# Performance work log

Measured on AMD Instinct MI355X. Metric: run time of the kernel, lower is better.

## Reference

```python
import jax, jax.numpy as jnp
import numpy as np

ALPHA = 0.2  # LeakyReLU negative slope
MASK_VAL = -1e9


def setup_inputs() -> dict:
    key = jax.random.key(0)
    k1, k2, k3, k4 = jax.random.split(key, 4)
    B, N, F_in, F_out = 8, 2048, 512, 512
    h = jax.random.normal(k1, (B, N, F_in), dtype=jnp.float32)
    adj = jax.random.randint(k2, (B, N, N), 0, 2, dtype=jnp.int32)
    # xavier_uniform with gain=1.414
    def xavier(k, shape, gain=1.414):
        fan_in, fan_out = shape[0], shape[1]
        bound = gain * np.sqrt(6.0 / (fan_in + fan_out))
        return jax.random.uniform(k, shape, jnp.float32, -bound, bound)
    W = xavier(k3, (F_in, F_out))
    a = xavier(k4, (2 * F_out, 1))
    return {"h": h, "adj": adj, "W": W, "a": a}


def reference(h, adj, W, a):
    # h: [B,N,Fin], adj: [B,N,N], W: [Fin,Fout], a: [2*Fout,1]
    Fout = W.shape[1]
    Wh = jnp.matmul(h, W)  # [B,N,Fout]
    # Split 'a' into source/target halves: concat([Wh_i, Wh_j]) @ a
    #   == (Wh_i @ a1) + (Wh_j @ a2), avoiding the O(N^2*2F) concat tensor.
    a1 = a[:Fout, 0]   # [Fout]
    a2 = a[Fout:, 0]   # [Fout]
    e_i = jnp.einsum('bnf,f->bn', Wh, a1)  # [B,N] score contribution of node i
    e_j = jnp.einsum('bnf,f->bn', Wh, a2)  # [B,N] score contribution of node j
    e = e_i[:, :, None] + e_j[:, None, :]  # [B,N,N]
    e = jax.nn.leaky_relu(e, negative_slope=ALPHA)
    e = jnp.where(adj == 0, MASK_VAL, e)
    attention = jax.nn.softmax(e, axis=2)  # [B,N,N]
    h_prime = jnp.matmul(attention, Wh)    # [B,N,Fout]
    return jax.nn.elu(h_prime)
```

## Files before the change

### kernel.cpp

```cpp
#include <hip/hip_runtime.h>
#include <hip/hip_bf16.h>

#define ALPHA 0.2f
#define LOG2E 1.44269504088896340736f

typedef float  f32x4 __attribute__((ext_vector_type(4)));
typedef float  f32x2 __attribute__((ext_vector_type(2)));
typedef int    i32x4 __attribute__((ext_vector_type(4)));
typedef int    i32x2 __attribute__((ext_vector_type(2)));

static __device__ __forceinline__ void mfma_bf16_16x16x32(f32x4& c, i32x4 a, i32x4 b) {
  asm("v_mfma_f32_16x16x32_bf16 %0, %1, %2, %0" : "+v"(c) : "v"(a), "v"(b));
}

static __device__ __forceinline__ unsigned short f2bf(float x) {
  __hip_bfloat16 b = __float2bfloat16(x);
  return *reinterpret_cast<unsigned short*>(&b);
}
static __device__ __forceinline__ unsigned int packbf2(float x, float y) {
  return (unsigned int)f2bf(x) | ((unsigned int)f2bf(y) << 16);
}
static __device__ __forceinline__ float dot4(f32x4 a, f32x4 b) {
  return a.x*b.x + a.y*b.y + a.z*b.z + a.w*b.w;
}

__global__ __launch_bounds__(256) void k_setup(const float* __restrict__ W, const float* __restrict__ a,
                                               unsigned short* __restrict__ wt,
                                               float* __restrict__ v1, float* __restrict__ v2) {
  const int bid = blockIdx.x, tid = threadIdx.x;
  __shared__ float S[32][33];
  if (bid < 256) {
    const int k0 = (bid >> 4) * 32, f0 = (bid & 15) * 32;
    const int r = tid >> 5, c = tid & 31;
    #pragma unroll
    for (int rr = r; rr < 32; rr += 8) S[rr][c] = W[(size_t)(k0 + rr) * 512 + f0 + c];
    __syncthreads();
    #pragma unroll
    for (int rr = r; rr < 32; rr += 8) wt[(size_t)(f0 + rr) * 512 + k0 + c] = f2bf(S[c][rr]);
  } else {
    const int kk = (bid - 256) * 4 + (tid >> 6);
    const int l = tid & 63;
    const float* wr = W + (size_t)kk * 512 + l * 8;
    f32x4 w0 = *(const f32x4*)(wr),           w1 = *(const f32x4*)(wr + 4);
    f32x4 p0 = *(const f32x4*)(a + l*8),      p1 = *(const f32x4*)(a + l*8 + 4);
    f32x4 q0 = *(const f32x4*)(a + 512 + l*8),q1 = *(const f32x4*)(a + 512 + l*8 + 4);
    float s1 = dot4(w0,p0) + dot4(w1,p1);
    float s2 = dot4(w0,q0) + dot4(w1,q1);
    #pragma unroll
    for (int off = 1; off < 64; off <<= 1) { s1 += __shfl_xor(s1, off); s2 += __shfl_xor(s2, off); }
    if (l == 0) { v1[kk] = s1; v2[kk] = s2; }
  }
}

__global__ __launch_bounds__(256) void k_ei_ej(const float* __restrict__ h,
                                               const float* __restrict__ v1, const float* __restrict__ v2,
                                               float* __restrict__ ei, float* __restrict__ ej) {
  const int row = blockIdx.x * 4 + (threadIdx.x >> 6);
  const int l = threadIdx.x & 63;
  const float* hr = h + (size_t)row * 512 + l * 8;
  f32x4 x0 = *(const f32x4*)hr,            x1 = *(const f32x4*)(hr + 4);
  f32x4 a0 = *(const f32x4*)(v1 + l*8),    a1 = *(const f32x4*)(v1 + l*8 + 4);
  f32x4 b0 = *(const f32x4*)(v2 + l*8),    b1 = *(const f32x4*)(v2 + l*8 + 4);
  float s1 = dot4(x0,a0) + dot4(x1,a1);
  float s2 = dot4(x0,b0) + dot4(x1,b1);
  #pragma unroll
  for (int off = 1; off < 64; off <<= 1) { s1 += __shfl_xor(s1, off); s2 += __shfl_xor(s2, off); }
  if (l == 0) { ei[row] = s1 * LOG2E; ej[row] = s2 * LOG2E; }
}

__global__ __launch_bounds__(512, 2) void k_gemm_wh(const float* __restrict__ h,
                                                    const unsigned short* __restrict__ wt,
                                                    unsigned short* __restrict__ whT) {
  const int tid = threadIdx.x;
  const int w = tid >> 6, l = tid & 63;
  const int i0g = blockIdx.x * 64;
  const int b = i0g >> 11;
  const int nb = i0g & 2047;
  __shared__ __align__(16) unsigned short Alds[2][4][64][8];

  const int sr = tid >> 3;
  const int sc = (tid & 7) * 4;
  const float* hrow = h + (size_t)(i0g + sr) * 512 + sc;

  const int fl = l & 15, kq = l >> 4;
  const unsigned short* wp[4];
  #pragma unroll
  for (int cf = 0; cf < 4; ++cf) {
    const int f = w*64 + cf*16 + fl;
    wp[cf] = wt + (size_t)f * 512 + kq * 8;
  }

  f32x4 acc[4][4];
  #pragma unroll
  for (int i = 0; i < 4; ++i)
    #pragma unroll
    for (int j = 0; j < 4; ++j) acc[i][j] = (f32x4){0.f,0.f,0.f,0.f};

  f32x4 hcur = *(const f32x4*)hrow;
  i32x4 bcur[4];
  #pragma unroll
  for (int cf = 0; cf < 4; ++cf) bcur[cf] = *(const i32x4*)(wp[cf]);

  for (int s = 0; s < 16; ++s) {
    const unsigned int lo = packbf2(hcur.x, hcur.y), hi = packbf2(hcur.z, hcur.w);
    *(i32x2*)&Alds[s & 1][sc >> 3][sr][sc & 7] = (i32x2){(int)lo, (int)hi};
    const int sn = (s < 15) ? s + 1 : 15;
    if (s < 15) hcur = *(const f32x4*)(hrow + sn * 32);
    __syncthreads();
    i32x4 bnxt[4];
    #pragma unroll
    for (int cf = 0; cf < 4; ++cf) bnxt[cf] = *(const i32x4*)(wp[cf] + sn * 32);
    i32x4 af[4];
    #pragma unroll
    for (int fr = 0; fr < 4; ++fr) af[fr] = *(const i32x4*)&Alds[s & 1][kq][fr*16 + fl][0];
    #pragma unroll
    for (int fr = 0; fr < 4; ++fr)
      #pragma unroll
      for (int cf = 0; cf < 4; ++cf)
        mfma_bf16_16x16x32(acc[fr][cf], af[fr], bcur[cf]);
    #pragma unroll
    for (int cf = 0; cf < 4; ++cf) bcur[cf] = bnxt[cf];
  }

  asm volatile("s_nop 7\ns_nop 7\ns_nop 7" :::);
  const int il0 = kq * 4;
  #pragma unroll
  for (int fr = 0; fr < 4; ++fr) {
    #pragma unroll
    for (int cf = 0; cf < 4; ++cf) {
      const f32x4 v = acc[fr][cf];
      const int f = w*64 + cf*16 + fl;
      const int n = nb + fr*16 + il0;
      unsigned long long pk = (unsigned long long)packbf2(v.x, v.y)
                            | ((unsigned long long)packbf2(v.z, v.w) << 32);
      *(unsigned long long*)(whT + (size_t)(b*512 + f) * 2048 + n) = pk;
    }
  }
}

__global__ __launch_bounds__(512, 2) void k_attn(const int* __restrict__ adj,
                                                 const unsigned short* __restrict__ whT,
                                                 const float* __restrict__ ei, const float* __restrict__ ej,
                                                 float* __restrict__ out) {
  const int tid = threadIdx.x;
  const int w = tid >> 6, l = tid & 63;
  const int bid = blockIdx.x;
  const int b = bid >> 5;
  const int i0 = (bid & 31) * 64;

  __shared__ __align__(16) unsigned short Plds[2][64][40];
  __shared__ __align__(16) float ejl[2048];
  __shared__ __align__(16) float eil[64];
  __shared__ __align__(16) float llds[64];

  for (int idx = tid; idx < 2048; idx += 512) ejl[idx] = ej[b*2048 + idx];
  if (tid < 64) eil[tid] = ei[b*2048 + i0 + tid];
  __syncthreads();

  const int r = tid >> 4, c2 = tid & 15;
  const float eir0 = eil[r], eir1 = eil[r + 32];
  const int* adj0 = adj + (size_t)(b*2048 + i0 + r) * 2048 + c2*2;
  const int* adj1 = adj0 + (size_t)32 * 2048;

  const int fl = l & 15, kq = l >> 4;
  const unsigned short* wp[4];
  #pragma unroll
  for (int cf = 0; cf < 4; ++cf) {
    const int f = w*64 + cf*16 + fl;
    wp[cf] = whT + (size_t)(b*512 + f) * 2048 + kq*8;
  }

  f32x4 acc[4][4];
  #pragma unroll
  for (int i = 0; i < 4; ++i)
    #pragma unroll
    for (int j = 0; j < 4; ++j) acc[i][j] = (f32x4){0.f,0.f,0.f,0.f};
  float sum0 = 0.f, sum1 = 0.f;

  i32x2 a0c = *(const i32x2*)(adj0);
  i32x2 a1c = *(const i32x2*)(adj1);
  i32x4 bcur[4];
  #pragma unroll
  for (int cf = 0; cf < 4; ++cf) bcur[cf] = *(const i32x4*)(wp[cf]);

  for (int t = 0; t < 64; ++t) {
    const int tn = (t < 63) ? t + 1 : 63;
    i32x2 a0n = *(const i32x2*)(adj0 + tn*32);
    i32x2 a1n = *(const i32x2*)(adj1 + tn*32);
    i32x4 bnxt[4];
    #pragma unroll
    for (int cf = 0; cf < 4; ++cf) bnxt[cf] = *(const i32x4*)(wp[cf] + tn*32);

    const f32x2 ejv = *(const f32x2*)&ejl[t*32 + c2*2];
    float e00 = eir0 + ejv.x, e01 = eir0 + ejv.y;
    float e10 = eir1 + ejv.x, e11 = eir1 + ejv.y;
    e00 = fmaxf(e00, ALPHA*e00); e01 = fmaxf(e01, ALPHA*e01);
    e10 = fmaxf(e10, ALPHA*e10); e11 = fmaxf(e11, ALPHA*e11);
    const float p00 = a0c.x ? __builtin_amdgcn_exp2f(e00) : 0.f;
    const float p01 = a0c.y ? __builtin_amdgcn_exp2f(e01) : 0.f;
    const float p10 = a1c.x ? __builtin_amdgcn_exp2f(e10) : 0.f;
    const float p11 = a1c.y ? __builtin_amdgcn_exp2f(e11) : 0.f;
    sum0 += p00 + p01; sum1 += p10 + p11;
    *(unsigned int*)&Plds[t & 1][r][c2*2]      = packbf2(p00, p01);
    *(unsigned int*)&Plds[t & 1][r + 32][c2*2] = packbf2(p10, p11);
    __syncthreads();

    i32x4 af[4];
    #pragma unroll
    for (int fr = 0; fr < 4; ++fr) af[fr] = *(const i32x4*)&Plds[t & 1][fr*16 + fl][kq*8];
    #pragma unroll
    for (int fr = 0; fr < 4; ++fr)
      #pragma unroll
      for (int cf = 0; cf < 4; ++cf)
        mfma_bf16_16x16x32(acc[fr][cf], af[fr], bcur[cf]);

    #pragma unroll
    for (int cf = 0; cf < 4; ++cf) bcur[cf] = bnxt[cf];
    a0c = a0n; a1c = a1n;
  }

  #pragma unroll
  for (int off = 1; off < 16; off <<= 1) { sum0 += __shfl_xor(sum0, off); sum1 += __shfl_xor(sum1, off); }
  if (c2 == 0) { llds[r] = sum0; llds[r + 32] = sum1; }
  __syncthreads();
  asm volatile("s_nop 7\ns_nop 7\ns_nop 7" :::);

  #pragma unroll
  for (int fr = 0; fr < 4; ++fr) {
    const f32x4 lv = *(const f32x4*)&llds[fr*16 + kq*4];
    f32x4 inv;
    inv.x = __builtin_amdgcn_rcpf(lv.x); inv.y = __builtin_amdgcn_rcpf(lv.y);
    inv.z = __builtin_amdgcn_rcpf(lv.z); inv.w = __builtin_amdgcn_rcpf(lv.w);
    #pragma unroll
    for (int cf = 0; cf < 4; ++cf) {
      const int f = w*64 + cf*16 + fl;
      float* op = out + (size_t)(b*2048 + i0 + fr*16 + kq*4) * 512 + f;
      const f32x4 v = acc[fr][cf];
      float o0 = v.x * inv.x; o0 = o0 > 0.f ? o0 : __expf(o0) - 1.f; op[0]    = o0;
      float o1 = v.y * inv.y; o1 = o1 > 0.f ? o1 : __expf(o1) - 1.f; op[512]  = o1;
      float o2 = v.z * inv.z; o2 = o2 > 0.f ? o2 : __expf(o2) - 1.f; op[1024] = o2;
      float o3 = v.w * inv.w; o3 = o3 > 0.f ? o3 : __expf(o3) - 1.f; op[1536] = o3;
    }
  }
}

extern "C" void kernel_launch(void* const* d_in, const int* in_sizes, int n_in,
                              void* d_out, int out_size, void* d_ws, size_t ws_size,
                              hipStream_t stream) {
  const float* h  = (const float*)d_in[0];
  const int*  adj = (const int*)d_in[1];
  const float* W  = (const float*)d_in[2];
  const float* a  = (const float*)d_in[3];
  float* out = (float*)d_out;
  char* ws = (char*)d_ws;
  unsigned short* wt  = (unsigned short*)(ws);
  unsigned short* whT = (unsigned short*)(ws + 524288);
  float* ei = (float*)(ws + 524288 + 16777216);
  float* ej = ei + 16384;
  float* v1 = ej + 16384;
  float* v2 = v1 + 512;

  hipLaunchKernelGGL(k_setup,  dim3(384),  dim3(256), 0, stream, W, a, wt, v1, v2);
  hipLaunchKernelGGL(k_ei_ej,  dim3(4096), dim3(256), 0, stream, h, v1, v2, ei, ej);
  hipLaunchKernelGGL(k_gemm_wh,dim3(256),  dim3(512), 0, stream, h, wt, whT);
  hipLaunchKernelGGL(k_attn,   dim3(256),  dim3(512), 0, stream, adj, whT, ei, ej, out);
}
```

Before: 318.7 us.

## Reassociate attention as (P·h)·W and pack adjacency into LDS bitmasks

The pipeline is reordered so attention multiplies the transposed bf16 copy of h directly, and the W projection runs afterwards as a separate GEMM with the ELU epilogue. This removes the up-front Wh GEMM and the O(N·F) Wh intermediate. The attention kernel now loads adjacency rows in bulk with nontemporal vector loads, compresses them to bitmasks in LDS, and computes probabilities directly in MFMA A-fragment registers, avoiding the per-step P round trip through LDS. ei/ej are fused into the transpose kernel using atomics, and a bf16 C1 intermediate adds an extra rounding step and extra traffic.

```diff
diff --git a/kernel.cpp b/kernel.cpp
--- a/kernel.cpp
+++ b/kernel.cpp
@@ -8,17 +8,19 @@
 typedef float  f32x2 __attribute__((ext_vector_type(2)));
 typedef int    i32x4 __attribute__((ext_vector_type(4)));
 typedef int    i32x2 __attribute__((ext_vector_type(2)));
+typedef unsigned int u32x2 __attribute__((ext_vector_type(2)));
 
 static __device__ __forceinline__ void mfma_bf16_16x16x32(f32x4& c, i32x4 a, i32x4 b) {
   asm("v_mfma_f32_16x16x32_bf16 %0, %1, %2, %0" : "+v"(c) : "v"(a), "v"(b));
 }
-
 static __device__ __forceinline__ unsigned short f2bf(float x) {
   __hip_bfloat16 b = __float2bfloat16(x);
   return *reinterpret_cast<unsigned short*>(&b);
 }
-static __device__ __forceinline__ unsigned int packbf2(float x, float y) {
-  return (unsigned int)f2bf(x) | ((unsigned int)f2bf(y) << 16);
+static __device__ __forceinline__ unsigned int cvtpk(float lo, float hi) {
+  unsigned int r;
+  asm("v_cvt_pk_bf16_f32 %0, %1, %2" : "=v"(r) : "v"(lo), "v"(hi));
+  return r;
 }
 static __device__ __forceinline__ float dot4(f32x4 a, f32x4 b) {
   return a.x*b.x + a.y*b.y + a.z*b.z + a.w*b.w;
@@ -26,7 +28,8 @@
 
 __global__ __launch_bounds__(256) void k_setup(const float* __restrict__ W, const float* __restrict__ a,
                                                unsigned short* __restrict__ wt,
-                                               float* __restrict__ v1, float* __restrict__ v2) {
+                                               float* __restrict__ v1, float* __restrict__ v2,
+                                               float* __restrict__ eiej) {
   const int bid = blockIdx.x, tid = threadIdx.x;
   __shared__ float S[32][33];
   if (bid < 256) {
@@ -37,191 +40,184 @@
     __syncthreads();
     #pragma unroll
     for (int rr = r; rr < 32; rr += 8) wt[(size_t)(f0 + rr) * 512 + k0 + c] = f2bf(S[c][rr]);
-  } else {
+  } else if (bid < 384) {
     const int kk = (bid - 256) * 4 + (tid >> 6);
     const int l = tid & 63;
     const float* wr = W + (size_t)kk * 512 + l * 8;
-    f32x4 w0 = *(const f32x4*)(wr),           w1 = *(const f32x4*)(wr + 4);
-    f32x4 p0 = *(const f32x4*)(a + l*8),      p1 = *(const f32x4*)(a + l*8 + 4);
-    f32x4 q0 = *(const f32x4*)(a + 512 + l*8),q1 = *(const f32x4*)(a + 512 + l*8 + 4);
+    f32x4 w0 = *(const f32x4*)(wr),            w1 = *(const f32x4*)(wr + 4);
+    f32x4 p0 = *(const f32x4*)(a + l*8),       p1 = *(const f32x4*)(a + l*8 + 4);
+    f32x4 q0 = *(const f32x4*)(a + 512 + l*8), q1 = *(const f32x4*)(a + 512 + l*8 + 4);
     float s1 = dot4(w0,p0) + dot4(w1,p1);
     float s2 = dot4(w0,q0) + dot4(w1,q1);
     #pragma unroll
     for (int off = 1; off < 64; off <<= 1) { s1 += __shfl_xor(s1, off); s2 += __shfl_xor(s2, off); }
-    if (l == 0) { v1[kk] = s1; v2[kk] = s2; }
-  }
-}
-
-__global__ __launch_bounds__(256) void k_ei_ej(const float* __restrict__ h,
-                                               const float* __restrict__ v1, const float* __restrict__ v2,
-                                               float* __restrict__ ei, float* __restrict__ ej) {
-  const int row = blockIdx.x * 4 + (threadIdx.x >> 6);
-  const int l = threadIdx.x & 63;
-  const float* hr = h + (size_t)row * 512 + l * 8;
-  f32x4 x0 = *(const f32x4*)hr,            x1 = *(const f32x4*)(hr + 4);
-  f32x4 a0 = *(const f32x4*)(v1 + l*8),    a1 = *(const f32x4*)(v1 + l*8 + 4);
-  f32x4 b0 = *(const f32x4*)(v2 + l*8),    b1 = *(const f32x4*)(v2 + l*8 + 4);
-  float s1 = dot4(x0,a0) + dot4(x1,a1);
-  float s2 = dot4(x0,b0) + dot4(x1,b1);
-  #pragma unroll
-  for (int off = 1; off < 64; off <<= 1) { s1 += __shfl_xor(s1, off); s2 += __shfl_xor(s2, off); }
-  if (l == 0) { ei[row] = s1 * LOG2E; ej[row] = s2 * LOG2E; }
-}
-
-__global__ __launch_bounds__(512, 2) void k_gemm_wh(const float* __restrict__ h,
-                                                    const unsigned short* __restrict__ wt,
-                                                    unsigned short* __restrict__ whT) {
+    if (l == 0) { v1[kk] = s1 * LOG2E; v2[kk] = s2 * LOG2E; }
+  } else {
+    const int idx = (bid - 384) * 1024 + tid * 4;
+    *(f32x4*)(eiej + idx) = (f32x4){0.f,0.f,0.f,0.f};
+  }
+}
+
+__global__ __launch_bounds__(256) void k_prep(const float* __restrict__ h,
+                                              const float* __restrict__ v1, const float* __restrict__ v2,
+                                              unsigned short* __restrict__ hT,
+                                              float* __restrict__ ei, float* __restrict__ ej) {
+  const int bid = blockIdx.x, tid = threadIdx.x;
+  const int ft = bid & 15, nt = (bid >> 4) & 63, b = bid >> 10;
+  __shared__ __align__(16) float S[32][36];
+
+  const int n_loc = tid >> 3, fq = (tid & 7) * 4;
+  const f32x4 v = __builtin_nontemporal_load(
+      (const f32x4*)(h + (size_t)(b*2048 + nt*32 + n_loc)*512 + ft*32 + fq));
+  *(f32x4*)&S[n_loc][fq] = v;
+
+  const f32x4 a1 = *(const f32x4*)(v1 + ft*32 + fq);
+  const f32x4 a2 = *(const f32x4*)(v2 + ft*32 + fq);
+  float s1 = dot4(v, a1), s2 = dot4(v, a2);
+  #pragma unroll
+  for (int off = 1; off < 8; off <<= 1) { s1 += __shfl_xor(s1, off); s2 += __shfl_xor(s2, off); }
+  if ((tid & 7) == 0) {
+    atomicAdd(&ei[b*2048 + nt*32 + n_loc], s1);
+    atomicAdd(&ej[b*2048 + nt*32 + n_loc], s2);
+  }
+  __syncthreads();
+
+  const int f_loc = tid >> 3, nq = (tid & 7) * 4;
+  u32x2 pk;
+  pk.x = cvtpk(S[nq+0][f_loc], S[nq+1][f_loc]);
+  pk.y = cvtpk(S[nq+2][f_loc], S[nq+3][f_loc]);
+  *(u32x2*)(hT + (size_t)(b*512 + ft*32 + f_loc)*2048 + nt*32 + nq) = pk;
+}
+
+__global__ __launch_bounds__(512, 2) void k_attn(const int* __restrict__ adj,
+                                                 const unsigned short* __restrict__ hT,
+                                                 const float* __restrict__ ei, const float* __restrict__ ej,
+                                                 unsigned short* __restrict__ C1) {
   const int tid = threadIdx.x;
   const int w = tid >> 6, l = tid & 63;
-  const int i0g = blockIdx.x * 64;
-  const int b = i0g >> 11;
-  const int nb = i0g & 2047;
-  __shared__ __align__(16) unsigned short Alds[2][4][64][8];
-
-  const int sr = tid >> 3;
-  const int sc = (tid & 7) * 4;
-  const float* hrow = h + (size_t)(i0g + sr) * 512 + sc;
-
   const int fl = l & 15, kq = l >> 4;
-  const unsigned short* wp[4];
-  #pragma unroll
-  for (int cf = 0; cf < 4; ++cf) {
-    const int f = w*64 + cf*16 + fl;
-    wp[cf] = wt + (size_t)f * 512 + kq * 8;
-  }
+  const int b = blockIdx.x & 7;
+  const int i0 = (blockIdx.x >> 3) * 64;
+
+  __shared__ __align__(16) float ejl[2048];
+  __shared__ __align__(16) unsigned char abits[2][64][64];
+  __shared__ __align__(16) float llds[64];
+
+  for (int idx = tid; idx < 2048; idx += 512) ejl[idx] = ej[b*2048 + idx];
+
+  float eir[4];
+  #pragma unroll
+  for (int fr = 0; fr < 4; ++fr) eir[fr] = ei[b*2048 + i0 + fr*16 + fl];
+
+  const unsigned short* bp[4];
+  #pragma unroll
+  for (int cf = 0; cf < 4; ++cf)
+    bp[cf] = hT + (size_t)(b*512 + w*64 + cf*16 + fl) * 2048 + kq*8;
+
+  const int srow0 = tid >> 4, srow1 = 32 + (tid >> 4), stw = tid & 15;
+  const int* agp0 = adj + (size_t)(b*2048 + i0 + srow0) * 2048 + stw*32;
+  const int* agp1 = adj + (size_t)(b*2048 + i0 + srow1) * 2048 + stw*32;
+  const int wa0 = srow0*64 + ((stw*4 + 4*srow0) & 63);
+  const int wa1 = srow1*64 + ((stw*4 + 4*srow1) & 63);
 
   f32x4 acc[4][4];
   #pragma unroll
   for (int i = 0; i < 4; ++i)
     #pragma unroll
     for (int j = 0; j < 4; ++j) acc[i][j] = (f32x4){0.f,0.f,0.f,0.f};
-
-  f32x4 hcur = *(const f32x4*)hrow;
-  i32x4 bcur[4];
-  #pragma unroll
-  for (int cf = 0; cf < 4; ++cf) bcur[cf] = *(const i32x4*)(wp[cf]);
-
-  for (int s = 0; s < 16; ++s) {
-    const unsigned int lo = packbf2(hcur.x, hcur.y), hi = packbf2(hcur.z, hcur.w);
-    *(i32x2*)&Alds[s & 1][sc >> 3][sr][sc & 7] = (i32x2){(int)lo, (int)hi};
-    const int sn = (s < 15) ? s + 1 : 15;
-    if (s < 15) hcur = *(const f32x4*)(hrow + sn * 32);
+  float s[4] = {0.f, 0.f, 0.f, 0.f};
+
+  i32x4 bcur[4], bnxt[4];
+  #pragma unroll
+  for (int cf = 0; cf < 4; ++cf) bcur[cf] = *(const i32x4*)(bp[cf]);
+
+  i32x4 va[16];
+  #pragma unroll
+  for (int q = 0; q < 8; ++q) {
+    va[q]   = __builtin_nontemporal_load((const i32x4*)(agp0 + q*4));
+    va[8+q] = __builtin_nontemporal_load((const i32x4*)(agp1 + q*4));
+  }
+  {
+    unsigned int b0 = 0, b1 = 0;
+    #pragma unroll
+    for (int q = 0; q < 8; ++q)
+      #pragma unroll
+      for (int e = 0; e < 4; ++e) {
+        b0 |= ((unsigned)va[q][e]   & 1u) << (q*4 + e);
+        b1 |= ((unsigned)va[8+q][e] & 1u) << (q*4 + e);
+      }
+    *(unsigned int*)(&abits[0][0][0] + wa0) = b0;
+    *(unsigned int*)(&abits[0][0][0] + wa1) = b1;
+  }
+  __syncthreads();
+
+  for (int c = 0; c < 4; ++c) {
+    const int cur = c & 1;
+    if (c < 3) {
+      const int jo = (c + 1) * 512;
+      #pragma unroll
+      for (int q = 0; q < 8; ++q) {
+        va[q]   = __builtin_nontemporal_load((const i32x4*)(agp0 + jo + q*4));
+        va[8+q] = __builtin_nontemporal_load((const i32x4*)(agp1 + jo + q*4));
+      }
+    }
+    for (int tl = 0; tl < 16; ++tl) {
+      const int t = c*16 + tl;
+      if (t < 63) {
+        #pragma unroll
+        for (int cf = 0; cf < 4; ++cf) bnxt[cf] = *(const i32x4*)(bp[cf] + (t+1)*32);
+      }
+      const f32x4 ej0 = *(const f32x4*)&ejl[t*32 + kq*8];
+      const f32x4 ej1 = *(const f32x4*)&ejl[t*32 + kq*8 + 4];
+      const int ao = (tl*4 + kq + 4*fl) & 63;
+      i32x4 af[4];
+      #pragma unroll
+      for (int fr = 0; fr < 4; ++fr) {
+        const unsigned int byt = abits[cur][fr*16 + fl][ao];
+        float p[8];
+        #pragma unroll
+        for (int e = 0; e < 8; ++e) {
+          float ee = eir[fr] + ((e < 4) ? ej0[e] : ej1[e-4]);
+          ee = fmaxf(ee, ALPHA * ee);
+          const float pv = __builtin_amdgcn_exp2f(ee);
+          p[e] = (byt & (1u << e)) ? pv : 0.f;
+          s[fr] += p[e];
+        }
+        af[fr] = (i32x4){ (int)cvtpk(p[0],p[1]), (int)cvtpk(p[2],p[3]),
+                          (int)cvtpk(p[4],p[5]), (int)cvtpk(p[6],p[7]) };
+      }
+      #pragma unroll
+      for (int fr = 0; fr < 4; ++fr)
+        #pragma unroll
+        for (int cf = 0; cf < 4; ++cf)
+          mfma_bf16_16x16x32(acc[fr][cf], af[fr], bcur[cf]);
+      #pragma unroll
+      for (int cf = 0; cf < 4; ++cf) bcur[cf] = bnxt[cf];
+    }
+    if (c < 3) {
+      unsigned int b0 = 0, b1 = 0;
+      #pragma unroll
+      for (int q = 0; q < 8; ++q)
+        #pragma unroll
+        for (int e = 0; e < 4; ++e) {
+          b0 |= ((unsigned)va[q][e]   & 1u) << (q*4 + e);
+          b1 |= ((unsigned)va[8+q][e] & 1u) << (q*4 + e);
+        }
+      *(unsigned int*)(&abits[cur ^ 1][0][0] + wa0) = b0;
+      *(unsigned int*)(&abits[cur ^ 1][0][0] + wa1) = b1;
+    }
     __syncthreads();
-    i32x4 bnxt[4];
-    #pragma unroll
-    for (int cf = 0; cf < 4; ++cf) bnxt[cf] = *(const i32x4*)(wp[cf] + sn * 32);
-    i32x4 af[4];
-    #pragma unroll
-    for (int fr = 0; fr < 4; ++fr) af[fr] = *(const i32x4*)&Alds[s & 1][kq][fr*16 + fl][0];
-    #pragma unroll
-    for (int fr = 0; fr < 4; ++fr)
-      #pragma unroll
-      for (int cf = 0; cf < 4; ++cf)
-        mfma_bf16_16x16x32(acc[fr][cf], af[fr], bcur[cf]);
-    #pragma unroll
-    for (int cf = 0; cf < 4; ++cf) bcur[cf] = bnxt[cf];
-  }
-
-  asm volatile("s_nop 7\ns_nop 7\ns_nop 7" :::);
-  const int il0 = kq * 4;
+  }
+
   #pragma unroll
   for (int fr = 0; fr < 4; ++fr) {
-    #pragma unroll
-    for (int cf = 0; cf < 4; ++cf) {
-      const f32x4 v = acc[fr][cf];
-      const int f = w*64 + cf*16 + fl;
-      const int n = nb + fr*16 + il0;
-      unsigned long long pk = (unsigned long long)packbf2(v.x, v.y)
-                            | ((unsigned long long)packbf2(v.z, v.w) << 32);
-      *(unsigned long long*)(whT + (size_t)(b*512 + f) * 2048 + n) = pk;
-    }
-  }
-}
-
-__global__ __launch_bounds__(512, 2) void k_attn(const int* __restrict__ adj,
-                                                 const unsigned short* __restrict__ whT,
-                                                 const float* __restrict__ ei, const float* __restrict__ ej,
-                                                 float* __restrict__ out) {
-  const int tid = threadIdx.x;
-  const int w = tid >> 6, l = tid & 63;
-  const int bid = blockIdx.x;
-  const int b = bid >> 5;
-  const int i0 = (bid & 31) * 64;
-
-  __shared__ __align__(16) unsigned short Plds[2][64][40];
-  __shared__ __align__(16) float ejl[2048];
-  __shared__ __align__(16) float eil[64];
-  __shared__ __align__(16) float llds[64];
-
-  for (int idx = tid; idx < 2048; idx += 512) ejl[idx] = ej[b*2048 + idx];
-  if (tid < 64) eil[tid] = ei[b*2048 + i0 + tid];
-  __syncthreads();
-
-  const int r = tid >> 4, c2 = tid & 15;
-  const float eir0 = eil[r], eir1 = eil[r + 32];
-  const int* adj0 = adj + (size_t)(b*2048 + i0 + r) * 2048 + c2*2;
-  const int* adj1 = adj0 + (size_t)32 * 2048;
-
-  const int fl = l & 15, kq = l >> 4;
-  const unsigned short* wp[4];
-  #pragma unroll
-  for (int cf = 0; cf < 4; ++cf) {
-    const int f = w*64 + cf*16 + fl;
-    wp[cf] = whT + (size_t)(b*512 + f) * 2048 + kq*8;
-  }
-
-  f32x4 acc[4][4];
-  #pragma unroll
-  for (int i = 0; i < 4; ++i)
-    #pragma unroll
-    for (int j = 0; j < 4; ++j) acc[i][j] = (f32x4){0.f,0.f,0.f,0.f};
-  float sum0 = 0.f, sum1 = 0.f;
-
-  i32x2 a0c = *(const i32x2*)(adj0);
-  i32x2 a1c = *(const i32x2*)(adj1);
-  i32x4 bcur[4];
-  #pragma unroll
-  for (int cf = 0; cf < 4; ++cf) bcur[cf] = *(const i32x4*)(wp[cf]);
-
-  for (int t = 0; t < 64; ++t) {
-    const int tn = (t < 63) ? t + 1 : 63;
-    i32x2 a0n = *(const i32x2*)(adj0 + tn*32);
-    i32x2 a1n = *(const i32x2*)(adj1 + tn*32);
-    i32x4 bnxt[4];
-    #pragma unroll
-    for (int cf = 0; cf < 4; ++cf) bnxt[cf] = *(const i32x4*)(wp[cf] + tn*32);
-
-    const f32x2 ejv = *(const f32x2*)&ejl[t*32 + c2*2];
-    float e00 = eir0 + ejv.x, e01 = eir0 + ejv.y;
-    float e10 = eir1 + ejv.x, e11 = eir1 + ejv.y;
-    e00 = fmaxf(e00, ALPHA*e00); e01 = fmaxf(e01, ALPHA*e01);
-    e10 = fmaxf(e10, ALPHA*e10); e11 = fmaxf(e11, ALPHA*e11);
-    const float p00 = a0c.x ? __builtin_amdgcn_exp2f(e00) : 0.f;
-    const float p01 = a0c.y ? __builtin_amdgcn_exp2f(e01) : 0.f;
-    const float p10 = a1c.x ? __builtin_amdgcn_exp2f(e10) : 0.f;
-    const float p11 = a1c.y ? __builtin_amdgcn_exp2f(e11) : 0.f;
-    sum0 += p00 + p01; sum1 += p10 + p11;
-    *(unsigned int*)&Plds[t & 1][r][c2*2]      = packbf2(p00, p01);
-    *(unsigned int*)&Plds[t & 1][r + 32][c2*2] = packbf2(p10, p11);
-    __syncthreads();
-
-    i32x4 af[4];
-    #pragma unroll
-    for (int fr = 0; fr < 4; ++fr) af[fr] = *(const i32x4*)&Plds[t & 1][fr*16 + fl][kq*8];
-    #pragma unroll
-    for (int fr = 0; fr < 4; ++fr)
-      #pragma unroll
-      for (int cf = 0; cf < 4; ++cf)
-        mfma_bf16_16x16x32(acc[fr][cf], af[fr], bcur[cf]);
-
-    #pragma unroll
-    for (int cf = 0; cf < 4; ++cf) bcur[cf] = bnxt[cf];
-    a0c = a0n; a1c = a1n;
-  }
-
-  #pragma unroll
-  for (int off = 1; off < 16; off <<= 1) { sum0 += __shfl_xor(sum0, off); sum1 += __shfl_xor(sum1, off); }
-  if (c2 == 0) { llds[r] = sum0; llds[r + 32] = sum1; }
+    s[fr] += __shfl_xor(s[fr], 16);
+    s[fr] += __shfl_xor(s[fr], 32);
+  }
+  if (w == 0 && kq == 0) {
+    #pragma unroll
+    for (int fr = 0; fr < 4; ++fr) llds[fr*16 + fl] = s[fr];
+  }
   __syncthreads();
   asm volatile("s_nop 7\ns_nop 7\ns_nop 7" :::);
 
@@ -234,14 +230,73 @@
     #pragma unroll
     for (int cf = 0; cf < 4; ++cf) {
       const int f = w*64 + cf*16 + fl;
-      float* op = out + (size_t)(b*2048 + i0 + fr*16 + kq*4) * 512 + f;
+      unsigned short* cp = C1 + (size_t)(b*2048 + i0 + fr*16 + kq*4) * 512 + f;
+      cp[0]    = f2bf(acc[fr][cf].x * inv.x);
+      cp[512]  = f2bf(acc[fr][cf].y * inv.y);
+      cp[1024] = f2bf(acc[fr][cf].z * inv.z);
+      cp[1536] = f2bf(acc[fr][cf].w * inv.w);
+    }
+  }
+}
+
+__global__ __launch_bounds__(512, 2) void k_gemm2(const unsigned short* __restrict__ C1,
+                                                  const unsigned short* __restrict__ wt,
+                                                  float* __restrict__ out) {
+  const int tid = threadIdx.x;
+  const int w = tid >> 6, l = tid & 63;
+  const int fl = l & 15, kq = l >> 4;
+  const int row0 = (blockIdx.x & 7) * 2048 + (blockIdx.x >> 3) * 64;
+
+  const unsigned short* ap[4];
+  const unsigned short* bp[4];
+  #pragma unroll
+  for (int fr = 0; fr < 4; ++fr) ap[fr] = C1 + (size_t)(row0 + fr*16 + fl)*512 + kq*8;
+  #pragma unroll
+  for (int cf = 0; cf < 4; ++cf) bp[cf] = wt + (size_t)(w*64 + cf*16 + fl)*512 + kq*8;
+
+  f32x4 acc[4][4];
+  #pragma unroll
+  for (int i = 0; i < 4; ++i)
+    #pragma unroll
+    for (int j = 0; j < 4; ++j) acc[i][j] = (f32x4){0.f,0.f,0.f,0.f};
+
+  i32x4 ac[4], bc[4], an[4], bn[4];
+  #pragma unroll
+  for (int x = 0; x < 4; ++x) { ac[x] = *(const i32x4*)(ap[x]); bc[x] = *(const i32x4*)(bp[x]); }
+
+  for (int sI = 0; sI < 16; ++sI) {
+    const int sn = (sI < 15) ? sI + 1 : 15;
+    #pragma unroll
+    for (int x = 0; x < 4; ++x) {
+      an[x] = *(const i32x4*)(ap[x] + sn*32);
+      bn[x] = *(const i32x4*)(bp[x] + sn*32);
+    }
+    #pragma unroll
+    for (int fr = 0; fr < 4; ++fr)
+      #pragma unroll
+      for (int cf = 0; cf < 4; ++cf)
+        mfma_bf16_16x16x32(acc[fr][cf], ac[fr], bc[cf]);
+    #pragma unroll
+    for (int x = 0; x < 4; ++x) { ac[x] = an[x]; bc[x] = bn[x]; }
+  }
+
+  asm volatile("s_nop 7\ns_nop 7\ns_nop 7" :::);
+  #pragma unroll
+  for (int fr = 0; fr < 4; ++fr)
+    #pragma unroll
+    for (int cf = 0; cf < 4; ++cf) {
+      const int f = w*64 + cf*16 + fl;
+      float* op = out + (size_t)(row0 + fr*16 + kq*4) * 512 + f;
       const f32x4 v = acc[fr][cf];
-      float o0 = v.x * inv.x; o0 = o0 > 0.f ? o0 : __expf(o0) - 1.f; op[0]    = o0;
-      float o1 = v.y * inv.y; o1 = o1 > 0.f ? o1 : __expf(o1) - 1.f; op[512]  = o1;
-      float o2 = v.z * inv.z; o2 = o2 > 0.f ? o2 : __expf(o2) - 1.f; op[1024] = o2;
-      float o3 = v.w * inv.w; o3 = o3 > 0.f ? o3 : __expf(o3) - 1.f; op[1536] = o3;
-    }
-  }
+      float o0 = v.x > 0.f ? v.x : __builtin_amdgcn_exp2f(v.x * LOG2E) - 1.f;
+      float o1 = v.y > 0.f ? v.y : __builtin_amdgcn_exp2f(v.y * LOG2E) - 1.f;
+      float o2 = v.z > 0.f ? v.z : __builtin_amdgcn_exp2f(v.z * LOG2E) - 1.f;
+      float o3 = v.w > 0.f ? v.w : __builtin_amdgcn_exp2f(v.w * LOG2E) - 1.f;
+      __builtin_nontemporal_store(o0, op);
+      __builtin_nontemporal_store(o1, op + 512);
+      __builtin_nontemporal_store(o2, op + 1024);
+      __builtin_nontemporal_store(o3, op + 1536);
+    }
 }
 
 extern "C" void kernel_launch(void* const* d_in, const int* in_sizes, int n_in,
@@ -253,15 +308,16 @@
   const float* a  = (const float*)d_in[3];
   float* out = (float*)d_out;
   char* ws = (char*)d_ws;
-  unsigned short* wt  = (unsigned short*)(ws);
-  unsigned short* whT = (unsigned short*)(ws + 524288);
-  float* ei = (float*)(ws + 524288 + 16777216);
-  float* ej = ei + 16384;
-  float* v1 = ej + 16384;
-  float* v2 = v1 + 512;
-
-  hipLaunchKernelGGL(k_setup,  dim3(384),  dim3(256), 0, stream, W, a, wt, v1, v2);
-  hipLaunchKernelGGL(k_ei_ej,  dim3(4096), dim3(256), 0, stream, h, v1, v2, ei, ej);
-  hipLaunchKernelGGL(k_gemm_wh,dim3(256),  dim3(512), 0, stream, h, wt, whT);
-  hipLaunchKernelGGL(k_attn,   dim3(256),  dim3(512), 0, stream, adj, whT, ei, ej, out);
-}
+  unsigned short* wt = (unsigned short*)(ws);
+  unsigned short* hT = (unsigned short*)(ws + 524288);
+  unsigned short* C1 = (unsigned short*)(ws + 17301504);
+  float* ei = (float*)(ws + 34078720);
+  float* ej = (float*)(ws + 34144256);
+  float* v1 = (float*)(ws + 34209792);
+  float* v2 = (float*)(ws + 34211840);
+
+  hipLaunchKernelGGL(k_setup, dim3(416),  dim3(256), 0, stream, W, a, wt, v1, v2, ei);
+  hipLaunchKernelGGL(k_prep,  dim3(8192), dim3(256), 0, stream, h, v1, v2, hT, ei, ej);
+  hipLaunchKernelGGL(k_attn,  dim3(256),  dim3(512), 0, stream, adj, hT, ei, ej, C1);
+  hipLaunchKernelGGL(k_gemm2, dim3(256),  dim3(512), 0, stream, C1, wt, out);
+}
```

Result: slower. 390.4 us (+22.5%).
